# Kernel optimization log

Hardware: AMD Instinct MI355X
Metric: run time of the kernel (lower is better)

## Reference

```python
import jax, jax.numpy as jnp
import numpy as np

N, L, S, C, H = 8, 1024, 1024, 512, 8
SCALE = float((C // H) ** 0.5)  # sqrt(64), as in source (based on embed_dim, not cat'd dim)


def _linear_params(key, c_in, c_out):
    kw, kb = jax.random.split(key)
    lim = 1.0 / np.sqrt(c_in)
    W = jax.random.uniform(kw, (c_out, c_in), jnp.float32, -lim, lim)
    b = jax.random.uniform(kb, (c_out,), jnp.float32, -lim, lim)
    return W, b


def setup_inputs() -> dict:
    key = jax.random.key(0)
    ks = jax.random.split(key, 12)
    inp = {
        'q_c': jax.random.normal(ks[0], (N, L, C), jnp.float32),
        'q_p': jax.random.normal(ks[1], (N, L, C), jnp.float32),
        'k_c': jax.random.normal(ks[2], (N, S, C), jnp.float32),
        'k_p': jax.random.normal(ks[3], (N, S, C), jnp.float32),
        'v': jax.random.normal(ks[4], (N, S, C), jnp.float32),
        'attn_mask': jax.random.normal(ks[5], (N, H, L, S), jnp.float32),
    }
    for i, name in enumerate(['qc', 'qp', 'kc', 'kp', 'v', 'o']):
        W, b = _linear_params(ks[6 + i], C, C)
        inp[f'W_{name}'] = W
        inp[f'b_{name}'] = b
    return inp


def _split_head(x, h):
    n, l, c = x.shape
    return x.reshape(n, l, h, c // h).transpose(0, 2, 1, 3)  # (N,H,L,c/h)


def reference(q_c, q_p, k_c, k_p, v, attn_mask,
              W_qc, b_qc, W_qp, b_qp, W_kc, b_kc, W_kp, b_kp, W_v, b_v, W_o, b_o):
    # dual projections + cat -> (N, L, 2C)
    q = jnp.concatenate([q_c @ W_qc.T + b_qc, q_p @ W_qp.T + b_qp], axis=-1)
    k = jnp.concatenate([k_c @ W_kc.T + b_kc, k_p @ W_kp.T + b_kp], axis=-1)
    vv = v @ W_v.T + b_v
    q = _split_head(q, H)   # (N,H,L,2C/H)
    k = _split_head(k, H)   # (N,H,S,2C/H)
    vv = _split_head(vv, H)  # (N,H,S,C/H)
    attn = jnp.einsum('nhld,nhsd->nhls', q / SCALE, k) + attn_mask
    attn = jax.nn.softmax(attn, axis=-1)
    out = jnp.einsum('nhls,nhsd->nhld', attn, vv)
    out = out.transpose(0, 2, 1, 3).reshape(N, L, C)
    return out @ W_o.T + b_o
```

## Files before the change

### kernel.cpp

```cpp
#include <hip/hip_runtime.h>
#include <hip/hip_bf16.h>

typedef __bf16 bf16;
typedef __bf16 bf16x8 __attribute__((ext_vector_type(8)));
typedef float  f32x4  __attribute__((ext_vector_type(4)));
typedef float  f32x2  __attribute__((ext_vector_type(2)));

#define LOG2E        1.4426950408889634f
#define QSCALE_LOG2E 0.18033688011112043f
#define DEFER_THR    20.0f

#define GLDS(g, l)                                                        \
  __builtin_amdgcn_global_load_lds(                                       \
      (const __attribute__((address_space(1))) void*)(g),                 \
      (__attribute__((address_space(3))) void*)(l), 16, 0, 0)

#define VMCNT_BAR(n) do {                                                 \
  asm volatile("s_waitcnt vmcnt(" #n ")" ::: "memory");                   \
  __builtin_amdgcn_s_barrier();                                           \
  __builtin_amdgcn_sched_barrier(0);                                      \
} while (0)

__device__ __forceinline__ void stage_f32_tile(const float* __restrict__ src, int ld,
                                               char* dst, int tid) {
  #pragma unroll
  for (int t = 0; t < 8; ++t) {
    int c8  = tid + t * 256;
    int row = c8 >> 4;
    int h8  = c8 & 15;
    const f32x4 v = *reinterpret_cast<const f32x4*>(src + row * ld + h8 * 4);
    union { bf16 h[4]; unsigned long long u; } pk;
    pk.h[0] = (bf16)v[0]; pk.h[1] = (bf16)v[1];
    pk.h[2] = (bf16)v[2]; pk.h[3] = (bf16)v[3];
    int byte = (row << 7) + ((((h8 >> 1) ^ (row & 7)) << 4) | ((h8 & 1) << 3));
    *reinterpret_cast<unsigned long long*>(dst + byte) = pk.u;
  }
}

__device__ __forceinline__ void stage_bf16_tile(const bf16* __restrict__ src, int ld,
                                                char* dst, int tid) {
  #pragma unroll
  for (int t = 0; t < 4; ++t) {
    int c   = tid + t * 256;
    int row = c >> 3;
    int ck  = c & 7;
    const bf16x8 v = *reinterpret_cast<const bf16x8*>(src + row * ld + ck * 8);
    int byte = (row << 7) + (((ck ^ (row & 7)) << 4));
    *reinterpret_cast<bf16x8*>(dst + byte) = v;
  }
}

__global__ __launch_bounds__(256) void proj_gemm(
    const float* __restrict__ qc, const float* __restrict__ qp,
    const float* __restrict__ kc, const float* __restrict__ kp,
    const float* __restrict__ vin,
    const float* __restrict__ Wqc, const float* __restrict__ bqc,
    const float* __restrict__ Wqp, const float* __restrict__ bqp,
    const float* __restrict__ Wkc, const float* __restrict__ bkc,
    const float* __restrict__ Wkp, const float* __restrict__ bkp,
    const float* __restrict__ Wv,  const float* __restrict__ bv,
    bf16* __restrict__ Qws, bf16* __restrict__ Kws, bf16* __restrict__ Vtws) {
  __shared__ __align__(16) bf16 lA[128 * 64];
  __shared__ __align__(16) bf16 lB[128 * 64];
  char* lAb = (char*)lA;
  char* lBb = (char*)lB;

  const int bx = blockIdx.x;
  const int g  = bx >> 8;
  const int mt = (bx & 255) >> 2;
  const int nt = bx & 3;

  const float *A, *W, *bias;
  if      (g == 0) { A = qc;  W = Wqc; bias = bqc; }
  else if (g == 1) { A = qp;  W = Wqp; bias = bqp; }
  else if (g == 2) { A = kc;  W = Wkc; bias = bkc; }
  else if (g == 3) { A = kp;  W = Wkp; bias = bkp; }
  else             { A = vin; W = Wv;  bias = bv;  }

  const int tid  = threadIdx.x;
  const int lane = tid & 63, wid = tid >> 6;
  const int wr = wid >> 1, wc = wid & 1;
  const int lrow = lane & 15, lgrp = lane >> 4;

  const float* Abase = A + (size_t)(mt * 128) * 512;
  const float* Wbase = W + (size_t)(nt * 128) * 512;

  const f32x4 fz = {0.f, 0.f, 0.f, 0.f};
  f32x4 acc[4][4];
  #pragma unroll
  for (int i = 0; i < 4; ++i)
    #pragma unroll
    for (int j = 0; j < 4; ++j) acc[i][j] = fz;

  for (int k0 = 0; k0 < 512; k0 += 64) {
    __syncthreads();
    stage_f32_tile(Abase + k0, 512, lAb, tid);
    stage_f32_tile(Wbase + k0, 512, lBb, tid);
    __syncthreads();
    #pragma unroll
    for (int kk = 0; kk < 2; ++kk) {
      bf16x8 af[4], bfr[4];
      #pragma unroll
      for (int mf = 0; mf < 4; ++mf) {
        int row  = wr * 64 + mf * 16 + lrow;
        int byte = (row << 7) + ((((kk << 2) | lgrp) ^ (row & 7)) << 4);
        af[mf] = *reinterpret_cast<const bf16x8*>(lAb + byte);
      }
      #pragma unroll
      for (int nf = 0; nf < 4; ++nf) {
        int row  = wc * 64 + nf * 16 + lrow;
        int byte = (row << 7) + ((((kk << 2) | lgrp) ^ (row & 7)) << 4);
        bfr[nf] = *reinterpret_cast<const bf16x8*>(lBb + byte);
      }
      #pragma unroll
      for (int mf = 0; mf < 4; ++mf)
        #pragma unroll
        for (int nf = 0; nf < 4; ++nf)
          acc[mf][nf] = __builtin_amdgcn_mfma_f32_16x16x32_bf16(
              af[mf], bfr[nf], acc[mf][nf], 0, 0, 0);
    }
  }

  float bcol[4];
  #pragma unroll
  for (int nf = 0; nf < 4; ++nf)
    bcol[nf] = bias[nt * 128 + wc * 64 + nf * 16 + lrow];

  #pragma unroll
  for (int mf = 0; mf < 4; ++mf) {
    #pragma unroll
    for (int nf = 0; nf < 4; ++nf) {
      #pragma unroll
      for (int r = 0; r < 4; ++r) {
        int grow = mt * 128 + wr * 64 + mf * 16 + lgrp * 4 + r;
        int col  = nt * 128 + wc * 64 + nf * 16 + lrow;
        float vv = acc[mf][nf][r] + bcol[nf];
        bf16 hb  = (bf16)vv;
        int n = grow >> 10, tt = grow & 1023;
        if (g < 2) {
          int j = (g << 9) + col;
          Qws[(size_t)((((n << 3) + (j >> 7)) << 10) | tt) * 128 + (j & 127)] = hb;
        } else if (g < 4) {
          int j = ((g - 2) << 9) + col;
          Kws[(size_t)((((n << 3) + (j >> 7)) << 10) | tt) * 128 + (j & 127)] = hb;
        } else {
          int h = col >> 6, d = col & 63;
          Vtws[(size_t)((((n << 3) + h) << 6) + d) * 1024 + tt] = hb;
        }
      }
    }
  }
}

__global__ __launch_bounds__(256) void attn_fwd(
    const bf16* __restrict__ Qws, const bf16* __restrict__ Kws,
    const bf16* __restrict__ Vtws, const float* __restrict__ mask,
    bf16* __restrict__ Ows) {
  __shared__ __align__(16) char Kl[3][8192];
  __shared__ __align__(16) char Vl[3][4096];
  __shared__ __align__(16) char Pl[4][1024];

  const int bx = blockIdx.x;
  const int nh = bx >> 4;
  const int qt = bx & 15;
  const int tid = threadIdx.x;
  const int lane = tid & 63, wid = tid >> 6;
  const int lrow = lane & 15, lgrp = lane >> 4;
  const int q0 = qt * 64 + wid * 16;

  const bf16* Qb = Qws + ((size_t)(nh * 1024 + q0 + lrow)) * 128 + lgrp * 8;
  bf16x8 qf[4];
  #pragma unroll
  for (int kk = 0; kk < 4; ++kk)
    qf[kk] = *reinterpret_cast<const bf16x8*>(Qb + kk * 32);

  const float* Mb = mask + ((size_t)(nh * 1024 + q0 + lgrp * 4)) * 1024 + 2 * lrow;

  const int kc0 = wid * 128 + lane;
  const int kr0 = kc0 >> 4, kd0 = kc0 & 15;
  const bf16* Kg0 = Kws + ((size_t)(nh * 1024 + kr0)) * 128 + (kd0 ^ ((kr0 >> 1) & 7)) * 8;
  const int kc1 = kc0 + 64;
  const int kr1 = kc1 >> 4, kd1 = kc1 & 15;
  const bf16* Kg1 = Kws + ((size_t)(nh * 1024 + kr1)) * 128 + (kd1 ^ ((kr1 >> 1) & 7)) * 8;
  const int vc  = wid * 64 + lane;
  const int vr  = vc >> 2, vs = vc & 3;
  const bf16* Vg = Vtws + ((size_t)(nh * 64 + vr)) * 1024 + vs * 8;

  char* Pb = &Pl[wid][0];

  const f32x4 fz = {0.f, 0.f, 0.f, 0.f};
  f32x4 oacc[4];
  #pragma unroll
  for (int dt = 0; dt < 4; ++dt) oacc[dt] = fz;
  float m2[4], lsum[4];
  #pragma unroll
  for (int r = 0; r < 4; ++r) { m2[r] = 0.f; lsum[r] = 0.f; }

  auto stageKV = [&](char* Ksg, char* Vsg, int sN) {
    GLDS(Kg0 + (size_t)sN * 128, Ksg + wid * 2048);
    GLDS(Kg1 + (size_t)sN * 128, Ksg + wid * 2048 + 1024);
    GLDS(Vg + sN,                Vsg + wid * 1024);
  };

  auto compute = [&](const char* Kb, const char* Vb, f32x2 (&MK)[4]) {
    bf16x8 kf0[4], kf1[4], vf[4];
    #pragma unroll
    for (int kk = 0; kk < 4; ++kk) {
      int cb = ((((kk << 2) | lgrp) ^ (lrow & 7)) << 4);
      kf0[kk] = *reinterpret_cast<const bf16x8*>(Kb + lrow * 512 + cb);
      kf1[kk] = *reinterpret_cast<const bf16x8*>(Kb + lrow * 512 + 256 + cb);
    }
    #pragma unroll
    for (int dt = 0; dt < 4; ++dt)
      vf[dt] = *reinterpret_cast<const bf16x8*>(Vb + (dt * 16 + lrow) * 64 + lgrp * 16);

    f32x4 sc0 = fz, sc1 = fz;
    __builtin_amdgcn_s_setprio(1);
    #pragma unroll
    for (int kk = 0; kk < 4; ++kk)
      sc0 = __builtin_amdgcn_mfma_f32_16x16x32_bf16(qf[kk], kf0[kk], sc0, 0, 0, 0);
    #pragma unroll
    for (int kk = 0; kk < 4; ++kk)
      sc1 = __builtin_amdgcn_mfma_f32_16x16x32_bf16(qf[kk], kf1[kk], sc1, 0, 0, 0);
    __builtin_amdgcn_s_setprio(0);

    float a0r[4], a1r[4];
    bool ok = true;
    #pragma unroll
    for (int r = 0; r < 4; ++r) {
      f32x2 mv = MK[r];
      a0r[r] = fmaf(sc0[r], QSCALE_LOG2E, mv.x * LOG2E);
      a1r[r] = fmaf(sc1[r], QSCALE_LOG2E, mv.y * LOG2E);
      ok &= (fmaxf(a0r[r], a1r[r]) <= m2[r] + DEFER_THR);
    }
    if (__builtin_expect(!__all(ok), 0)) {
      #pragma unroll
      for (int r = 0; r < 4; ++r) {
        float tv = fmaxf(a0r[r], a1r[r]);
        tv = fmaxf(tv, __shfl_xor(tv, 1));
        tv = fmaxf(tv, __shfl_xor(tv, 2));
        tv = fmaxf(tv, __shfl_xor(tv, 4));
        tv = fmaxf(tv, __shfl_xor(tv, 8));
        float mn = fmaxf(m2[r], tv);
        float corr = exp2f(m2[r] - mn);
        m2[r] = mn;
        lsum[r] *= corr;
        #pragma unroll
        for (int dt = 0; dt < 4; ++dt) oacc[dt][r] *= corr;
      }
    }
    #pragma unroll
    for (int r = 0; r < 4; ++r) {
      float e0 = exp2f(a0r[r] - m2[r]);
      float e1 = exp2f(a1r[r] - m2[r]);
      lsum[r] += e0 + e1;
      union { bf16 h[2]; unsigned u; } pk;
      pk.h[0] = (bf16)e0; pk.h[1] = (bf16)e1;
      int row = lgrp * 4 + r;
      int byte = row * 64 + ((((lrow >> 2) ^ (row & 3)) << 4) | ((lrow & 3) << 2));
      *reinterpret_cast<unsigned*>(Pb + byte) = pk.u;
    }
    __builtin_amdgcn_wave_barrier();
    __builtin_amdgcn_sched_barrier(0);
    bf16x8 pf = *reinterpret_cast<const bf16x8*>(
        Pb + lrow * 64 + ((lgrp ^ (lrow & 3)) << 4));

    __builtin_amdgcn_s_setprio(1);
    #pragma unroll
    for (int dt = 0; dt < 4; ++dt)
      oacc[dt] = __builtin_amdgcn_mfma_f32_16x16x32_bf16(pf, vf[dt], oacc[dt], 0, 0, 0);
    __builtin_amdgcn_s_setprio(0);
  };

  auto step_main = [&](const char* Kb, const char* Vb, char* Ksg, char* Vsg,
                       int sN, f32x2 (&MK)[4]) {
    stageKV(Ksg, Vsg, sN);
    f32x2 mnew[4];
    #pragma unroll
    for (int r = 0; r < 4; ++r)
      mnew[r] = *reinterpret_cast<const f32x2*>(Mb + (size_t)r * 1024 + sN);
    compute(Kb, Vb, MK);
    #pragma unroll
    for (int r = 0; r < 4; ++r) MK[r] = mnew[r];
  };

  char *k0 = &Kl[0][0], *k1 = &Kl[1][0], *k2 = &Kl[2][0];
  char *v0 = &Vl[0][0], *v1 = &Vl[1][0], *v2 = &Vl[2][0];
  char *kc_ = k0, *kn_ = k1, *kf_ = k2;
  char *vc_ = v0, *vn_ = v1, *vf_ = v2;

  stageKV(kc_, vc_, 0);
  stageKV(kn_, vn_, 32);
  f32x2 mX[4], mY[4];
  #pragma unroll
  for (int r = 0; r < 4; ++r) {
    mX[r] = *reinterpret_cast<const f32x2*>(Mb + (size_t)r * 1024);
    mY[r] = *reinterpret_cast<const f32x2*>(Mb + (size_t)r * 1024 + 32);
  }
  VMCNT_BAR(8);

  for (int tt = 0; tt < 15; ++tt) {
    int s0 = tt * 64;
    step_main(kc_, vc_, kf_, vf_, s0 + 64, mX);
    VMCNT_BAR(11);
    step_main(kn_, vn_, kc_, vc_, s0 + 96, mY);
    VMCNT_BAR(11);
    char* t1 = kc_; kc_ = kf_; kf_ = kn_; kn_ = t1;
    char* t2 = vc_; vc_ = vf_; vf_ = vn_; vn_ = t2;
  }

  compute(kc_, vc_, mX);
  VMCNT_BAR(4);
  compute(kn_, vn_, mY);

  #pragma unroll
  for (int r = 0; r < 4; ++r) {
    float ss = lsum[r];
    ss += __shfl_xor(ss, 1);
    ss += __shfl_xor(ss, 2);
    ss += __shfl_xor(ss, 4);
    ss += __shfl_xor(ss, 8);
    lsum[r] = 1.0f / ss;
  }

  const int n = nh >> 3, h = nh & 7;
  bf16* Ob = Ows + ((size_t)(n * 1024 + q0 + lgrp * 4)) * 512 + h * 64 + lrow;
  #pragma unroll
  for (int dt = 0; dt < 4; ++dt)
    #pragma unroll
    for (int r = 0; r < 4; ++r)
      Ob[(size_t)r * 512 + dt * 16] = (bf16)(oacc[dt][r] * lsum[r]);
}

__global__ __launch_bounds__(256) void out_gemm(
    const bf16* __restrict__ Ows, const float* __restrict__ Wo,
    const float* __restrict__ bo, float* __restrict__ out) {
  __shared__ __align__(16) bf16 lA[128 * 64];
  __shared__ __align__(16) bf16 lB[128 * 64];
  char* lAb = (char*)lA;
  char* lBb = (char*)lB;

  const int bx = blockIdx.x;
  const int mt = bx >> 2;
  const int nt = bx & 3;
  const int tid = threadIdx.x;
  const int lane = tid & 63, wid = tid >> 6;
  const int wr = wid >> 1, wc = wid & 1;
  const int lrow = lane & 15, lgrp = lane >> 4;

  const bf16*  Abase = Ows + (size_t)(mt * 128) * 512;
  const float* Wbase = Wo  + (size_t)(nt * 128) * 512;

  const f32x4 fz = {0.f, 0.f, 0.f, 0.f};
  f32x4 acc[4][4];
  #pragma unroll
  for (int i = 0; i < 4; ++i)
    #pragma unroll
    for (int j = 0; j < 4; ++j) acc[i][j] = fz;

  for (int k0 = 0; k0 < 512; k0 += 64) {
    __syncthreads();
    stage_bf16_tile(Abase + k0, 512, lAb, tid);
    stage_f32_tile(Wbase + k0, 512, lBb, tid);
    __syncthreads();
    #pragma unroll
    for (int kk = 0; kk < 2; ++kk) {
      bf16x8 af[4], bfr[4];
      #pragma unroll
      for (int mf = 0; mf < 4; ++mf) {
        int row  = wr * 64 + mf * 16 + lrow;
        int byte = (row << 7) + ((((kk << 2) | lgrp) ^ (row & 7)) << 4);
        af[mf] = *reinterpret_cast<const bf16x8*>(lAb + byte);
      }
      #pragma unroll
      for (int nf = 0; nf < 4; ++nf) {
        int row  = wc * 64 + nf * 16 + lrow;
        int byte = (row << 7) + ((((kk << 2) | lgrp) ^ (row & 7)) << 4);
        bfr[nf] = *reinterpret_cast<const bf16x8*>(lBb + byte);
      }
      #pragma unroll
      for (int mf = 0; mf < 4; ++mf)
        #pragma unroll
        for (int nf = 0; nf < 4; ++nf)
          acc[mf][nf] = __builtin_amdgcn_mfma_f32_16x16x32_bf16(
              af[mf], bfr[nf], acc[mf][nf], 0, 0, 0);
    }
  }

  float bcol[4];
  #pragma unroll
  for (int nf = 0; nf < 4; ++nf)
    bcol[nf] = bo[nt * 128 + wc * 64 + nf * 16 + lrow];

  #pragma unroll
  for (int mf = 0; mf < 4; ++mf) {
    #pragma unroll
    for (int nf = 0; nf < 4; ++nf) {
      #pragma unroll
      for (int r = 0; r < 4; ++r) {
        int grow = mt * 128 + wr * 64 + mf * 16 + lgrp * 4 + r;
        int col  = nt * 128 + wc * 64 + nf * 16 + lrow;
        out[(size_t)grow * 512 + col] = acc[mf][nf][r] + bcol[nf];
      }
    }
  }
}

extern "C" void kernel_launch(void* const* d_in, const int* in_sizes, int n_in,
                              void* d_out, int out_size, void* d_ws, size_t ws_size,
                              hipStream_t stream) {
  const float* qc   = (const float*)d_in[0];
  const float* qp   = (const float*)d_in[1];
  const float* kc   = (const float*)d_in[2];
  const float* kp   = (const float*)d_in[3];
  const float* vin  = (const float*)d_in[4];
  const float* mask = (const float*)d_in[5];
  const float* Wqc  = (const float*)d_in[6];
  const float* bqc  = (const float*)d_in[7];
  const float* Wqp  = (const float*)d_in[8];
  const float* bqp  = (const float*)d_in[9];
  const float* Wkc  = (const float*)d_in[10];
  const float* bkc  = (const float*)d_in[11];
  const float* Wkp  = (const float*)d_in[12];
  const float* bkp  = (const float*)d_in[13];
  const float* Wv   = (const float*)d_in[14];
  const float* bv   = (const float*)d_in[15];
  const float* Wo   = (const float*)d_in[16];
  const float* bo   = (const float*)d_in[17];

  bf16* Qws  = (bf16*)d_ws;
  bf16* Kws  = Qws  + (size_t)8 * 1024 * 1024;
  bf16* Vtws = Kws  + (size_t)8 * 1024 * 1024;
  bf16* Ows  = Vtws + (size_t)4 * 1024 * 1024;

  proj_gemm<<<dim3(1280), dim3(256), 0, stream>>>(
      qc, qp, kc, kp, vin, Wqc, bqc, Wqp, bqp, Wkc, bkc, Wkp, bkp, Wv, bv,
      Qws, Kws, Vtws);
  attn_fwd<<<dim3(1024), dim3(256), 0, stream>>>(Qws, Kws, Vtws, mask, Ows);
  out_gemm<<<dim3(256), dim3(256), 0, stream>>>(Ows, Wo, bo, (float*)d_out);
}
```

Measured before the change: 196.8 us.

## Stage attention mask tiles through LDS with async global-to-LDS loads

The attention kernel now fetches the fp32 mask with per-block global_load_lds into a triple-buffered LDS ring, two tiles ahead of use. Each lane previously issued its own strided register loads of mask values. K/V staging drops from a triple buffer to a double buffer, and the loop is restructured into a single-stage pipeline with a waitcnt/barrier per 32-key step. The aim is to coalesce the mask stream and hide its latency better. In exchange it uses more LDS per block, which may reduce occupancy, and adds more barriers per iteration.

```diff
diff --git a/kernel.cpp b/kernel.cpp
--- a/kernel.cpp
+++ b/kernel.cpp
@@ -156,8 +156,9 @@
     const bf16* __restrict__ Qws, const bf16* __restrict__ Kws,
     const bf16* __restrict__ Vtws, const float* __restrict__ mask,
     bf16* __restrict__ Ows) {
-  __shared__ __align__(16) char Kl[3][8192];
-  __shared__ __align__(16) char Vl[3][4096];
+  __shared__ __align__(16) char Kl[2][8192];
+  __shared__ __align__(16) char Vl[2][4096];
+  __shared__ __align__(16) char Ml[3][8192];
   __shared__ __align__(16) char Pl[4][1024];
 
   const int bx = blockIdx.x;
@@ -173,8 +174,6 @@
   #pragma unroll
   for (int kk = 0; kk < 4; ++kk)
     qf[kk] = *reinterpret_cast<const bf16x8*>(Qb + kk * 32);
-
-  const float* Mb = mask + ((size_t)(nh * 1024 + q0 + lgrp * 4)) * 1024 + 2 * lrow;
 
   const int kc0 = wid * 128 + lane;
   const int kr0 = kc0 >> 4, kd0 = kc0 & 15;
@@ -185,6 +184,10 @@
   const int vc  = wid * 64 + lane;
   const int vr  = vc >> 2, vs = vc & 3;
   const bf16* Vg = Vtws + ((size_t)(nh * 64 + vr)) * 1024 + vs * 8;
+  const float* Mblk = mask + ((size_t)(nh * 1024) + qt * 64) * 1024;
+  const int mc0 = wid * 64 + lane;
+  const float* Mg0 = Mblk + (size_t)(mc0 >> 3) * 1024 + (mc0 & 7) * 4;
+  const float* Mg1 = Mg0 + (size_t)32 * 1024;
 
   char* Pb = &Pl[wid][0];
 
@@ -201,8 +204,12 @@
     GLDS(Kg1 + (size_t)sN * 128, Ksg + wid * 2048 + 1024);
     GLDS(Vg + sN,                Vsg + wid * 1024);
   };
-
-  auto compute = [&](const char* Kb, const char* Vb, f32x2 (&MK)[4]) {
+  auto stageM = [&](char* Msg, int sN) {
+    GLDS(Mg0 + sN, Msg + wid * 1024);
+    GLDS(Mg1 + sN, Msg + 4096 + wid * 1024);
+  };
+
+  auto compute = [&](const char* Kb, const char* Vb, const char* Mb) {
     bf16x8 kf0[4], kf1[4], vf[4];
     #pragma unroll
     for (int kk = 0; kk < 4; ++kk) {
@@ -213,6 +220,12 @@
     #pragma unroll
     for (int dt = 0; dt < 4; ++dt)
       vf[dt] = *reinterpret_cast<const bf16x8*>(Vb + (dt * 16 + lrow) * 64 + lgrp * 16);
+    f32x2 mk[4];
+    #pragma unroll
+    for (int r = 0; r < 4; ++r) {
+      int qrow = wid * 16 + lgrp * 4 + r;
+      mk[r] = *reinterpret_cast<const f32x2*>(Mb + qrow * 128 + lrow * 8);
+    }
 
     f32x4 sc0 = fz, sc1 = fz;
     __builtin_amdgcn_s_setprio(1);
@@ -228,9 +241,8 @@
     bool ok = true;
     #pragma unroll
     for (int r = 0; r < 4; ++r) {
-      f32x2 mv = MK[r];
-      a0r[r] = fmaf(sc0[r], QSCALE_LOG2E, mv.x * LOG2E);
-      a1r[r] = fmaf(sc1[r], QSCALE_LOG2E, mv.y * LOG2E);
+      a0r[r] = fmaf(sc0[r], QSCALE_LOG2E, mk[r].x * LOG2E);
+      a1r[r] = fmaf(sc1[r], QSCALE_LOG2E, mk[r].y * LOG2E);
       ok &= (fmaxf(a0r[r], a1r[r]) <= m2[r] + DEFER_THR);
     }
     if (__builtin_expect(!__all(ok), 0)) {
@@ -272,46 +284,30 @@
     __builtin_amdgcn_s_setprio(0);
   };
 
-  auto step_main = [&](const char* Kb, const char* Vb, char* Ksg, char* Vsg,
-                       int sN, f32x2 (&MK)[4]) {
-    stageKV(Ksg, Vsg, sN);
-    f32x2 mnew[4];
-    #pragma unroll
-    for (int r = 0; r < 4; ++r)
-      mnew[r] = *reinterpret_cast<const f32x2*>(Mb + (size_t)r * 1024 + sN);
-    compute(Kb, Vb, MK);
-    #pragma unroll
-    for (int r = 0; r < 4; ++r) MK[r] = mnew[r];
-  };
-
-  char *k0 = &Kl[0][0], *k1 = &Kl[1][0], *k2 = &Kl[2][0];
-  char *v0 = &Vl[0][0], *v1 = &Vl[1][0], *v2 = &Vl[2][0];
-  char *kc_ = k0, *kn_ = k1, *kf_ = k2;
-  char *vc_ = v0, *vn_ = v1, *vf_ = v2;
-
-  stageKV(kc_, vc_, 0);
-  stageKV(kn_, vn_, 32);
-  f32x2 mX[4], mY[4];
-  #pragma unroll
-  for (int r = 0; r < 4; ++r) {
-    mX[r] = *reinterpret_cast<const f32x2*>(Mb + (size_t)r * 1024);
-    mY[r] = *reinterpret_cast<const f32x2*>(Mb + (size_t)r * 1024 + 32);
-  }
-  VMCNT_BAR(8);
-
-  for (int tt = 0; tt < 15; ++tt) {
-    int s0 = tt * 64;
-    step_main(kc_, vc_, kf_, vf_, s0 + 64, mX);
-    VMCNT_BAR(11);
-    step_main(kn_, vn_, kc_, vc_, s0 + 96, mY);
-    VMCNT_BAR(11);
-    char* t1 = kc_; kc_ = kf_; kf_ = kn_; kn_ = t1;
-    char* t2 = vc_; vc_ = vf_; vf_ = vn_; vn_ = t2;
-  }
-
-  compute(kc_, vc_, mX);
-  VMCNT_BAR(4);
-  compute(kn_, vn_, mY);
+  char *kcur = &Kl[0][0], *knxt = &Kl[1][0];
+  char *vcur = &Vl[0][0], *vnxt = &Vl[1][0];
+  char *m0p = &Ml[0][0], *m1p = &Ml[1][0], *m2p = &Ml[2][0];
+
+  stageM(m0p, 0);
+  stageKV(kcur, vcur, 0);
+  stageM(m1p, 32);
+  VMCNT_BAR(2);
+
+  for (int t = 0; t < 30; ++t) {
+    stageKV(knxt, vnxt, (t + 1) * 32);
+    stageM(m2p, (t + 2) * 32);
+    compute(kcur, vcur, m0p);
+    VMCNT_BAR(2);
+    char* tp;
+    tp = kcur; kcur = knxt; knxt = tp;
+    tp = vcur; vcur = vnxt; vnxt = tp;
+    tp = m0p; m0p = m1p; m1p = m2p; m2p = tp;
+  }
+
+  stageKV(knxt, vnxt, 31 * 32);
+  compute(kcur, vcur, m0p);
+  VMCNT_BAR(0);
+  compute(knxt, vnxt, m1p);
 
   #pragma unroll
   for (int r = 0; r < 4; ++r) {
```

After: 199.8 us. Within noise of the previous version (+1.5%).
